# Optimization experiments

Measured on AMD Instinct MI355X. Metric: run time of the kernel, lower is better.

Reference implementation:

```python
import jax, jax.numpy as jnp
import numpy as np

T, N, B, D = 64, 8, 128, 128      # time, n_agents, batch, obs_dim
H, S, K, A = 512, 64, 16, 16       # hidden_dim, subtask_dim, num_subtasks, action_dim
NB = N * B


def setup_inputs() -> dict:
    key = jax.random.key(0)
    ks = jax.random.split(key, 16)
    r = lambda i, shape: jax.random.normal(ks[i], shape, jnp.float32) * 0.02
    return dict(
        h1=jnp.zeros((NB, H), jnp.float32),
        h2=jnp.zeros((NB, H), jnp.float32),
        obs=jax.random.normal(ks[0], (T, N, B, D), jnp.float32),
        done=jax.random.bernoulli(ks[1], 0.05, (T, NB)),
        W_embed=r(2, (D, H)), b_embed=jnp.zeros((H,), jnp.float32),
        Wi1=r(3, (H, 3 * H)), bi1=jnp.zeros((3 * H,), jnp.float32),
        Wh1=r(4, (H, 3 * H)), bhn1=jnp.zeros((H,), jnp.float32),
        W_sub=r(5, (H, S)), b_sub=jnp.zeros((S,), jnp.float32),
        W_e1=r(6, (K, S)), b_e1=jnp.zeros((S,), jnp.float32),
        W_e2=r(7, (S, S)), b_e2=jnp.zeros((S,), jnp.float32),
        W_pol=r(8, (D, H)), b_pol=jnp.zeros((H,), jnp.float32),
        Wi2=r(9, (H, 3 * H)), bi2=jnp.zeros((3 * H,), jnp.float32),
        Wh2=r(10, (H, 3 * H)), bhn2=jnp.zeros((H,), jnp.float32),
        W_w1=r(11, (S, H * A)), b_w1=jnp.zeros((H * A,), jnp.float32),
        W_b1=r(12, (S, A)), b_b1=jnp.zeros((A,), jnp.float32),
    )


def _gru(h0, xs, dones, Wi, bi, Wh, bhn):
    """Flax GRUCell with per-step reset-to-zero carry (ScannedRNN)."""
    def step(h, inp):
        x, d = inp
        h = jnp.where(d[:, None], 0.0, h)          # reset carry on done
        gi = x @ Wi + bi                            # (NB, 3H): ir|iz|in
        gh = h @ Wh                                 # (NB, 3H): hr|hz|hn (hn bias separate)
        ir, iz, inn = jnp.split(gi, 3, axis=-1)
        hr, hz, hn = jnp.split(gh, 3, axis=-1)
        rg = jax.nn.sigmoid(ir + hr)
        zg = jax.nn.sigmoid(iz + hz)
        ng = jnp.tanh(inn + rg * (hn + bhn))
        hnew = (1.0 - zg) * ng + zg * h
        return hnew, hnew
    return jax.lax.scan(step, h0, (xs, dones))


def reference(h1, h2, obs, done, W_embed, b_embed, Wi1, bi1, Wh1, bhn1,
              W_sub, b_sub, W_e1, b_e1, W_e2, b_e2, W_pol, b_pol,
              Wi2, bi2, Wh2, bhn2, W_w1, b_w1, W_b1, b_b1):
    t, n, b, _ = obs.shape
    obs_f = obs.reshape(t, n * b, -1)                       # (T, NB, D)

    # agent embedding branch + GRU 1
    ae = jax.nn.relu(obs_f @ W_embed + b_embed)             # (T, NB, H)
    hT1, y1 = _gru(h1, ae, done, Wi1, bi1, Wh1, bhn1)
    ae2 = y1 @ W_sub + b_sub                                # (T, NB, S)
    ae2 = jnp.transpose(ae2.reshape(t, n, b, S), (0, 2, 1, 3))  # (T, B, N, S)

    # subtask embedding: input is eye(K), identical over (t, b) -> compute once
    e = jnp.tanh(jax.nn.relu(jnp.eye(K, dtype=obs.dtype) @ W_e1 + b_e1) @ W_e2 + b_e2)  # (K, S)
    subtask_embed = jnp.broadcast_to(e, (t, b, K, S))

    subtask_logits = jnp.einsum('tbns,ks->tbnk', ae2, e)    # (T, B, N, K)
    subtask_prob = jax.nn.one_hot(jnp.argmax(subtask_logits, axis=-1), K, dtype=obs.dtype)  # eval path

    # subtask policy branch + GRU 2
    sp = jax.nn.relu(obs_f @ W_pol + b_pol)                 # (T, NB, H)
    hT2, y2 = _gru(h2, sp, done, Wi2, bi2, Wh2, bhn2)

    # hypernetwork: _subtask_embed = stop_grad(subtask_embed[:, 0]) == e (time-invariant)
    e_sg = jax.lax.stop_gradient(e)
    w1 = (e_sg @ W_w1 + b_w1).reshape(K, H, A)              # (K, H, A)
    b1 = e_sg @ W_b1 + b_b1                                 # (K, A)

    # equivalent to the repeated-w1 batched matmul, without materializing (T,NB*K,H,A)
    q = jnp.einsum('tbh,kha->tbka', y2, w1) + b1            # (T, NB, K, A), NB in (N,B)-major order

    # faithful to original: prob flattened (B,N)-major vs q flattened (N,B)-major
    prob_flat = subtask_prob.reshape(t, b * n, K)
    q_vals = jnp.einsum('tbk,tbka->tba', prob_flat, q)      # (T, NB, A)

    return ((hT1, hT2), q_vals, subtask_logits, subtask_embed)
```

## Files before the change

kernel.cpp:

```cpp
#include <hip/hip_runtime.h>
#include <hip/hip_bf16.h>
#include <math.h>

#define TT 64
#define NN 8
#define BB 128
#define DD 128
#define HH 512
#define SS 64
#define KK 16
#define AA 16
#define NB 1024
#define H3 (3*HH)

typedef float f4v  __attribute__((ext_vector_type(4)));
typedef float f16v __attribute__((ext_vector_type(16)));
typedef short bf16x8 __attribute__((ext_vector_type(8)));

__device__ __forceinline__ float sigm(float x){ return 1.0f/(1.0f+expf(-x)); }
__device__ __forceinline__ unsigned short f2bf(float f){
  unsigned u = __float_as_uint(f);
  u += 0x7FFF + ((u >> 16) & 1);
  return (unsigned short)(u >> 16);
}
__device__ __forceinline__ float bf2f(unsigned short h){
  return __uint_as_float(((unsigned)h) << 16);
}

__global__ __launch_bounds__(256) void k_detect(const unsigned char* __restrict__ raw,
                                                int* __restrict__ flag)
{
  __shared__ int cA, cB;
  if (threadIdx.x == 0){ cA = 0; cB = 0; }
  __syncthreads();
  int a = 0, b = 0;
  for (int i = threadIdx.x; i < TT*NB; i += 256){
    unsigned char v = raw[i];
    if (v > 1) a++;
    if ((i & 3) != 0 && v != 0) b++;
  }
  atomicAdd(&cA, a); atomicAdd(&cB, b);
  __syncthreads();
  if (threadIdx.x == 0) *flag = (cB == 0) ? 0 : (cA == 0 ? 1 : 2);
}

__global__ __launch_bounds__(256) void k_mask(const unsigned char* __restrict__ raw,
                                              const int* __restrict__ flag,
                                              float* __restrict__ mask)
{
  int i = blockIdx.x*256 + threadIdx.x;
  if (i >= TT*NB) return;
  int f = *flag;
  int v;
  if (f == 1)      v = (int)raw[i];
  else if (f == 0) v = ((const int*)raw)[i];
  else             v = (((const float*)raw)[i] != 0.0f);
  mask[i] = v ? 0.f : 1.f;
}


__global__ __launch_bounds__(256) void k_e(const float* __restrict__ W_e1, const float* __restrict__ b_e1,
                                           const float* __restrict__ W_e2, const float* __restrict__ b_e2,
                                           float* __restrict__ e_out)
{
  __shared__ float r1[KK*SS];
  int tid = threadIdx.x;
  for (int i=0;i<4;++i){ int l = tid + i*256; float v = W_e1[l] + b_e1[l & 63]; r1[l] = v > 0.f ? v : 0.f; }
  __syncthreads();
  for (int i=0;i<4;++i){
    int l = tid + i*256; int k = l >> 6, s = l & 63;
    float acc = b_e2[s];
    #pragma unroll 8
    for (int sp=0; sp<64; ++sp) acc += r1[k*64+sp] * W_e2[sp*64 + s];
    e_out[l] = tanhf(acc);
  }
}

__global__ __launch_bounds__(256) void k_w1b1(const float* __restrict__ e, const float* __restrict__ W_w1,
                                              const float* __restrict__ b_w1, const float* __restrict__ W_b1,
                                              const float* __restrict__ b_b1, float* __restrict__ w1,
                                              float* __restrict__ b1)
{
  __shared__ float es[KK*SS];
  int tid = threadIdx.x;
  for (int i=0;i<4;++i) es[tid + i*256] = e[tid + i*256];
  __syncthreads();
  for (int i=0;i<4;++i){
    int l = blockIdx.x*1024 + tid + i*256;
    int k = l >> 13, m = l & 8191;
    float acc = b_w1[m];
    #pragma unroll 8
    for (int s=0;s<64;++s) acc += es[k*64+s] * W_w1[(size_t)s*8192 + m];
    w1[l] = acc;
  }
  if (blockIdx.x == 0){
    int k = tid >> 4, a = tid & 15;
    float acc = b_b1[a];
    #pragma unroll 8
    for (int s=0;s<64;++s) acc += es[k*64+s] * W_b1[s*16 + a];
    b1[tid] = acc;
  }
}

__global__ __launch_bounds__(256) void k_se(const float* __restrict__ e, float* __restrict__ outse)
{
  __shared__ float4 es[256];
  es[threadIdx.x] = ((const float4*)e)[threadIdx.x];
  __syncthreads();
  const int total4 = TT*BB*KK*SS/4;
  for (int i = blockIdx.x*256 + threadIdx.x; i < total4; i += gridDim.x*256)
    ((float4*)outse)[i] = es[i & 255];
}

__global__ void k_copy(const float* __restrict__ src, float* __restrict__ dst, int n4)
{
  int i = blockIdx.x*blockDim.x + threadIdx.x;
  if (i < n4) ((float4*)dst)[i] = ((const float4*)src)[i];
}

__global__ void k_merge(const unsigned short* __restrict__ h, const unsigned short* __restrict__ l,
                        float* __restrict__ o, int n8)
{
  int i = blockIdx.x*blockDim.x + threadIdx.x;
  if (i >= n8) return;
  uint4 vh = *(const uint4*)&h[(size_t)i*8];
  uint4 vl = *(const uint4*)&l[(size_t)i*8];
  const unsigned short* ph = (const unsigned short*)&vh;
  const unsigned short* pl = (const unsigned short*)&vl;
  float4 o0, o1;
  o0.x = bf2f(ph[0])+bf2f(pl[0]); o0.y = bf2f(ph[1])+bf2f(pl[1]);
  o0.z = bf2f(ph[2])+bf2f(pl[2]); o0.w = bf2f(ph[3])+bf2f(pl[3]);
  o1.x = bf2f(ph[4])+bf2f(pl[4]); o1.y = bf2f(ph[5])+bf2f(pl[5]);
  o1.z = bf2f(ph[6])+bf2f(pl[6]); o1.w = bf2f(ph[7])+bf2f(pl[7]);
  float4* d = (float4*)&o[(size_t)i*8];
  d[0] = o0; d[1] = o1;
}

__global__ void k_expand(const unsigned short* __restrict__ src, float* __restrict__ dst, int n8)
{
  int i = blockIdx.x*blockDim.x + threadIdx.x;
  if (i >= n8) return;
  uint4 v = *(const uint4*)&src[(size_t)i*8];
  const unsigned short* p = (const unsigned short*)&v;
  float4 o0 = make_float4(bf2f(p[0]),bf2f(p[1]),bf2f(p[2]),bf2f(p[3]));
  float4 o1 = make_float4(bf2f(p[4]),bf2f(p[5]),bf2f(p[6]),bf2f(p[7]));
  float4* d = (float4*)&dst[(size_t)i*8];
  d[0] = o0; d[1] = o1;
}

__global__ void k_cast_bf16(const float* __restrict__ src, unsigned short* __restrict__ dst, int n8)
{
  int i = blockIdx.x*blockDim.x + threadIdx.x;
  if (i >= n8) return;
  const float4* s = (const float4*)(src + (size_t)i*8);
  float4 a = s[0], b = s[1];
  union { unsigned short u[8]; uint4 v; } p;
  p.u[0]=f2bf(a.x); p.u[1]=f2bf(a.y); p.u[2]=f2bf(a.z); p.u[3]=f2bf(a.w);
  p.u[4]=f2bf(b.x); p.u[5]=f2bf(b.y); p.u[6]=f2bf(b.z); p.u[7]=f2bf(b.w);
  *(uint4*)&dst[(size_t)i*8] = p.v;
}

__global__ __launch_bounds__(256) void k_tsplit(const float* __restrict__ W,
                                                unsigned short* __restrict__ WTh,
                                                unsigned short* __restrict__ WTl,
                                                int Kd, int Nc)
{
  __shared__ float t[32][33];
  int n0 = blockIdx.x * 32;
  int k0 = blockIdx.y * 32;
  int c = threadIdx.x & 31, r8 = threadIdx.x >> 5;
  for (int i=0;i<4;++i){
    int r = r8 + i*8;
    t[r][c] = W[(size_t)(k0+r)*Nc + n0 + c];
  }
  __syncthreads();
  for (int i=0;i<4;++i){
    int nr = r8 + i*8;
    float v = t[c][nr];
    unsigned short hi = f2bf(v);
    WTh[(size_t)(n0+nr)*Kd + k0 + c] = hi;
    WTl[(size_t)(n0+nr)*Kd + k0 + c] = f2bf(v - bf2f(hi));
  }
}

__global__ void k_split_cast(const float* __restrict__ src,
                             unsigned short* __restrict__ dh,
                             unsigned short* __restrict__ dl, int n8)
{
  int i = blockIdx.x*blockDim.x + threadIdx.x;
  if (i >= n8) return;
  const float4* s = (const float4*)(src + (size_t)i*8);
  float4 a = s[0], b = s[1];
  float x[8] = {a.x,a.y,a.z,a.w,b.x,b.y,b.z,b.w};
  union { unsigned short u[8]; uint4 v; } ph, pl;
  #pragma unroll
  for (int j=0;j<8;++j){
    unsigned short hi = f2bf(x[j]);
    ph.u[j] = hi;
    pl.u[j] = f2bf(x[j] - bf2f(hi));
  }
  *(uint4*)&dh[(size_t)i*8] = ph.v;
  *(uint4*)&dl[(size_t)i*8] = pl.v;
}

template<int KD, int SPLIT, int NTILE, int RELU, int OUTMODE>
__global__ __launch_bounds__(256) void mfma_gemm(
    const unsigned short* Ah, const unsigned short* Al,
    const unsigned short* Bh, const unsigned short* Bl,
    const float* __restrict__ bias,
    float* C, unsigned short* Chi, unsigned short* Clo, int Nstride)
{
  constexpr int NFC = NTILE/16;
  __shared__ __align__(16) unsigned short AsH[128*40];
  __shared__ __align__(16) unsigned short BsH[NTILE*40];
  __shared__ __align__(16) unsigned short AsL[SPLIT ? 128*40 : 8];
  __shared__ __align__(16) unsigned short BsL[SPLIT ? NTILE*40 : 8];
  int tid = threadIdx.x;
  int w = tid >> 6, l = tid & 63;
  int lr = l & 15, lk = (l >> 4) * 8, lq = l >> 4;
  int rowBase = blockIdx.y * 128, colBase = blockIdx.x * NTILE;
  f4v acc[2][NFC];
  f4v z = {0.f,0.f,0.f,0.f};
  #pragma unroll
  for (int i=0;i<2;++i)
    #pragma unroll
    for (int j=0;j<NFC;++j) acc[i][j] = z;

  for (int k0 = 0; k0 < KD; k0 += 32){
    {
      int r = tid >> 1, half = tid & 1;
      size_t src = (size_t)(rowBase + r)*KD + k0 + half*16;
      bf16x8* dA = (bf16x8*)&AsH[r*40 + half*16];
      dA[0] = *(const bf16x8*)&Ah[src];
      dA[1] = *(const bf16x8*)&Ah[src + 8];
      if (SPLIT){
        bf16x8* dL = (bf16x8*)&AsL[r*40 + half*16];
        dL[0] = *(const bf16x8*)&Al[src];
        dL[1] = *(const bf16x8*)&Al[src + 8];
      }
    }
    if (NTILE == 128){
      int r = tid >> 1, half = tid & 1;
      size_t src = (size_t)(colBase + r)*KD + k0 + half*16;
      bf16x8* dB = (bf16x8*)&BsH[r*40 + half*16];
      dB[0] = *(const bf16x8*)&Bh[src];
      dB[1] = *(const bf16x8*)&Bh[src + 8];
      if (SPLIT){
        bf16x8* dL = (bf16x8*)&BsL[r*40 + half*16];
        dL[0] = *(const bf16x8*)&Bl[src];
        dL[1] = *(const bf16x8*)&Bl[src + 8];
      }
    } else {
      int r = tid >> 2, q = tid & 3;
      size_t src = (size_t)(colBase + r)*KD + k0 + q*8;
      *(bf16x8*)&BsH[r*40 + q*8] = *(const bf16x8*)&Bh[src];
      if (SPLIT)
        *(bf16x8*)&BsL[r*40 + q*8] = *(const bf16x8*)&Bl[src];
    }
    __syncthreads();
    bf16x8 aH0 = *(const bf16x8*)&AsH[(w*32 + lr)*40 + lk];
    bf16x8 aH1 = *(const bf16x8*)&AsH[(w*32 + 16 + lr)*40 + lk];
    bf16x8 aL0, aL1;
    if (SPLIT){
      aL0 = *(const bf16x8*)&AsL[(w*32 + lr)*40 + lk];
      aL1 = *(const bf16x8*)&AsL[(w*32 + 16 + lr)*40 + lk];
    }
    #pragma unroll
    for (int fc=0; fc<NFC; ++fc){
      bf16x8 bH = *(const bf16x8*)&BsH[(fc*16 + lr)*40 + lk];
      acc[0][fc] = __builtin_amdgcn_mfma_f32_16x16x32_bf16(aH0, bH, acc[0][fc], 0,0,0);
      acc[1][fc] = __builtin_amdgcn_mfma_f32_16x16x32_bf16(aH1, bH, acc[1][fc], 0,0,0);
      if (SPLIT){
        bf16x8 bL = *(const bf16x8*)&BsL[(fc*16 + lr)*40 + lk];
        acc[0][fc] = __builtin_amdgcn_mfma_f32_16x16x32_bf16(aH0, bL, acc[0][fc], 0,0,0);
        acc[1][fc] = __builtin_amdgcn_mfma_f32_16x16x32_bf16(aH1, bL, acc[1][fc], 0,0,0);
        acc[0][fc] = __builtin_amdgcn_mfma_f32_16x16x32_bf16(aL0, bH, acc[0][fc], 0,0,0);
        acc[1][fc] = __builtin_amdgcn_mfma_f32_16x16x32_bf16(aL1, bH, acc[1][fc], 0,0,0);
      }
    }
    __syncthreads();
  }
  #pragma unroll
  for (int fr=0; fr<2; ++fr){
    #pragma unroll
    for (int fc=0; fc<NFC; ++fc){
      int col = colBase + fc*16 + lr;
      float bv = bias[col];
      #pragma unroll
      for (int r=0;r<4;++r){
        int row = rowBase + w*32 + fr*16 + lq*4 + r;
        float v = acc[fr][fc][r] + bv;
        if (RELU) v = v > 0.f ? v : 0.f;
        size_t o = (size_t)row*Nstride + col;
        if (OUTMODE == 0) C[o] = v;
        else if (OUTMODE == 1) Chi[o] = f2bf(v);
        else {
          unsigned short hi = f2bf(v);
          Chi[o] = hi;
          Clo[o] = f2bf(v - bf2f(hi));
        }
      }
    }
  }
}

__global__ __launch_bounds__(256) void gru_step_mix5(
    const unsigned short* __restrict__ hp1h, const unsigned short* __restrict__ hp1l,
    const unsigned short* __restrict__ hp2b,
    const float* __restrict__ gi1, const float* __restrict__ gi2,
    const unsigned short* __restrict__ Wh1TH, const unsigned short* __restrict__ Wh1TL,
    const unsigned short* __restrict__ Wh2T,
    const float* __restrict__ bhn1, const float* __restrict__ bhn2,
    const float* __restrict__ mask_t,
    unsigned short* __restrict__ y2b,
    unsigned short* __restrict__ y1h, unsigned short* __restrict__ y1l)
{
  extern __shared__ __align__(16) char smem[];
  int bid = blockIdx.x;
  int tid = threadIdx.x;
  int w = tid >> 6, l = tid & 63;
  int rf = w & 1, hc = w >> 1;
  int lc = l & 31, lh = l >> 5;
  int sr = tid >> 2, sg = tid & 3;
  int gru = bid & 1, sub = bid >> 1;
  int ct = sub & 7, rt = sub >> 3;
  int rowBase = rt << 6, colBase = ct << 6;
  int capchunk = ct*2 + hc;
  bool keep = mask_t[rowBase + sr] != 0.f;
  f16v z16 = {0,0,0,0,0,0,0,0,0,0,0,0,0,0,0,0};
  uint4 zero4 = {0,0,0,0};

  if (gru == 0){
    f16v acc[3] = {z16, z16, z16};
    float hval[16];
    uint4 pA;
    bf16x8 pB[3];
    pA = *(const uint4*)&hp2b[(size_t)(rowBase + sr)*HH + sg*8];
    #pragma unroll
    for (int i=0;i<3;++i){
      int unit = i*256 + tid, brow = unit >> 2, q = unit & 3;
      int g = brow >> 6, c = brow & 63;
      pB[i] = *(const bf16x8*)&Wh2T[(size_t)(g*HH + colBase + c)*HH + q*8];
    }
    {
      unsigned short* As0 = (unsigned short*)smem;
      unsigned short* Bs0 = As0 + 64*40;
      *(uint4*)&As0[sr*40 + sg*8] = keep ? pA : zero4;
      #pragma unroll
      for (int i=0;i<3;++i){
        int unit = i*256 + tid, brow = unit >> 2, q = unit & 3;
        *(bf16x8*)&Bs0[brow*40 + q*8] = pB[i];
      }
    }
    pA = *(const uint4*)&hp2b[(size_t)(rowBase + sr)*HH + 32 + sg*8];
    #pragma unroll
    for (int i=0;i<3;++i){
      int unit = i*256 + tid, brow = unit >> 2, q = unit & 3;
      int g = brow >> 6, c = brow & 63;
      pB[i] = *(const bf16x8*)&Wh2T[(size_t)(g*HH + colBase + c)*HH + 32 + q*8];
    }
    __syncthreads();
    for (int ck = 0; ck < 16; ++ck){
      unsigned short* Asc = (unsigned short*)(smem + (ck&1)*20480);
      unsigned short* Bsc = Asc + 64*40;
      if (ck < 15){
        unsigned short* Asn = (unsigned short*)(smem + ((ck+1)&1)*20480);
        unsigned short* Bsn = Asn + 64*40;
        *(uint4*)&Asn[sr*40 + sg*8] = keep ? pA : zero4;
        #pragma unroll
        for (int i=0;i<3;++i){
          int unit = i*256 + tid, brow = unit >> 2, q = unit & 3;
          *(bf16x8*)&Bsn[brow*40 + q*8] = pB[i];
        }
      }
      if (ck < 14){
        int k0 = (ck+2)*32;
        pA = *(const uint4*)&hp2b[(size_t)(rowBase + sr)*HH + k0 + sg*8];
        #pragma unroll
        for (int i=0;i<3;++i){
          int unit = i*256 + tid, brow = unit >> 2, q = unit & 3;
          int g = brow >> 6, c = brow & 63;
          pB[i] = *(const bf16x8*)&Wh2T[(size_t)(g*HH + colBase + c)*HH + k0 + q*8];
        }
      }
      if (ck == capchunk){
        #pragma unroll
        for (int r=0;r<16;++r){
          int rl = rf*32 + (r&3) + 8*(r>>2) + 4*lh;
          hval[r] = bf2f(Asc[rl*40 + lc]);
        }
      }
      #pragma unroll
      for (int kc=0;kc<32;kc+=16){
        bf16x8 a = *(const bf16x8*)&Asc[(rf*32 + lc)*40 + kc + lh*8];
        #pragma unroll
        for (int g=0; g<3; ++g){
          bf16x8 b = *(const bf16x8*)&Bsc[(g*64 + hc*32 + lc)*40 + kc + lh*8];
          acc[g] = __builtin_amdgcn_mfma_f32_32x32x16_bf16(a, b, acc[g], 0,0,0);
        }
      }
      __syncthreads();
    }
    int col = colBase + hc*32 + lc;
    float bn = bhn2[col];
    #pragma unroll
    for (int r=0;r<16;++r){
      int row = rowBase + rf*32 + (r&3) + 8*(r>>2) + 4*lh;
      size_t gb = (size_t)row*H3 + col;
      float g_r = __builtin_nontemporal_load(&gi2[gb]);
      float g_z = __builtin_nontemporal_load(&gi2[gb + HH]);
      float g_n = __builtin_nontemporal_load(&gi2[gb + 2*HH]);
      float rg = sigm(g_r + acc[0][r]);
      float zg = sigm(g_z + acc[1][r]);
      float ng = tanhf(g_n + rg*(acc[2][r] + bn));
      float o  = (1.f - zg)*ng + zg*hval[r];
      y2b[(size_t)row*HH + col] = f2bf(o);
    }
  } else {
    f16v acc[3] = {z16, z16, z16};
    float hval[16];
    uint4 pAh, pAl;
    bf16x8 pBH[3], pBL[3];
    pAh = *(const uint4*)&hp1h[(size_t)(rowBase + sr)*HH + sg*8];
    pAl = *(const uint4*)&hp1l[(size_t)(rowBase + sr)*HH + sg*8];
    #pragma unroll
    for (int i=0;i<3;++i){
      int unit = i*256 + tid, brow = unit >> 2, q = unit & 3;
      int g = brow >> 6, c = brow & 63;
      size_t src = (size_t)(g*HH + colBase + c)*HH + q*8;
      pBH[i] = *(const bf16x8*)&Wh1TH[src];
      pBL[i] = *(const bf16x8*)&Wh1TL[src];
    }
    {
      unsigned short* AsH0 = (unsigned short*)smem;
      unsigned short* AsL0 = AsH0 + 64*40;
      unsigned short* BsH0 = AsL0 + 64*40;
      unsigned short* BsL0 = BsH0 + 192*40;
      *(uint4*)&AsH0[sr*40 + sg*8] = keep ? pAh : zero4;
      *(uint4*)&AsL0[sr*40 + sg*8] = keep ? pAl : zero4;
      #pragma unroll
      for (int i=0;i<3;++i){
        int unit = i*256 + tid, brow = unit >> 2, q = unit & 3;
        *(bf16x8*)&BsH0[brow*40 + q*8] = pBH[i];
        *(bf16x8*)&BsL0[brow*40 + q*8] = pBL[i];
      }
    }
    pAh = *(const uint4*)&hp1h[(size_t)(rowBase + sr)*HH + 32 + sg*8];
    pAl = *(const uint4*)&hp1l[(size_t)(rowBase + sr)*HH + 32 + sg*8];
    #pragma unroll
    for (int i=0;i<3;++i){
      int unit = i*256 + tid, brow = unit >> 2, q = unit & 3;
      int g = brow >> 6, c = brow & 63;
      size_t src = (size_t)(g*HH + colBase + c)*HH + 32 + q*8;
      pBH[i] = *(const bf16x8*)&Wh1TH[src];
      pBL[i] = *(const bf16x8*)&Wh1TL[src];
    }
    __syncthreads();
    for (int ck = 0; ck < 16; ++ck){
      unsigned short* AsHc = (unsigned short*)(smem + (ck&1)*40960);
      unsigned short* AsLc = AsHc + 64*40;
      unsigned short* BsHc = AsLc + 64*40;
      unsigned short* BsLc = BsHc + 192*40;
      if (ck < 15){
        unsigned short* AsHn = (unsigned short*)(smem + ((ck+1)&1)*40960);
        unsigned short* AsLn = AsHn + 64*40;
        unsigned short* BsHn = AsLn + 64*40;
        unsigned short* BsLn = BsHn + 192*40;
        *(uint4*)&AsHn[sr*40 + sg*8] = keep ? pAh : zero4;
        *(uint4*)&AsLn[sr*40 + sg*8] = keep ? pAl : zero4;
        #pragma unroll
        for (int i=0;i<3;++i){
          int unit = i*256 + tid, brow = unit >> 2, q = unit & 3;
          *(bf16x8*)&BsHn[brow*40 + q*8] = pBH[i];
          *(bf16x8*)&BsLn[brow*40 + q*8] = pBL[i];
        }
      }
      if (ck < 14){
        int k0 = (ck+2)*32;
        pAh = *(const uint4*)&hp1h[(size_t)(rowBase + sr)*HH + k0 + sg*8];
        pAl = *(const uint4*)&hp1l[(size_t)(rowBase + sr)*HH + k0 + sg*8];
        #pragma unroll
        for (int i=0;i<3;++i){
          int unit = i*256 + tid, brow = unit >> 2, q = unit & 3;
          int g = brow >> 6, c = brow & 63;
          size_t src = (size_t)(g*HH + colBase + c)*HH + k0 + q*8;
          pBH[i] = *(const bf16x8*)&Wh1TH[src];
          pBL[i] = *(const bf16x8*)&Wh1TL[src];
        }
      }
      if (ck == capchunk){
        #pragma unroll
        for (int r=0;r<16;++r){
          int rl = rf*32 + (r&3) + 8*(r>>2) + 4*lh;
          hval[r] = bf2f(AsHc[rl*40 + lc]) + bf2f(AsLc[rl*40 + lc]);
        }
      }
      #pragma unroll
      for (int kc=0;kc<32;kc+=16){
        bf16x8 aH = *(const bf16x8*)&AsHc[(rf*32 + lc)*40 + kc + lh*8];
        bf16x8 aL = *(const bf16x8*)&AsLc[(rf*32 + lc)*40 + kc + lh*8];
        #pragma unroll
        for (int g=0; g<3; ++g){
          int brow = (g*64 + hc*32 + lc)*40 + kc + lh*8;
          bf16x8 bH = *(const bf16x8*)&BsHc[brow];
          bf16x8 bL = *(const bf16x8*)&BsLc[brow];
          acc[g] = __builtin_amdgcn_mfma_f32_32x32x16_bf16(aH, bH, acc[g], 0,0,0);
          acc[g] = __builtin_amdgcn_mfma_f32_32x32x16_bf16(aH, bL, acc[g], 0,0,0);
          acc[g] = __builtin_amdgcn_mfma_f32_32x32x16_bf16(aL, bH, acc[g], 0,0,0);
        }
      }
      __syncthreads();
    }
    int col = colBase + hc*32 + lc;
    float bn = bhn1[col];
    #pragma unroll
    for (int r=0;r<16;++r){
      int row = rowBase + rf*32 + (r&3) + 8*(r>>2) + 4*lh;
      size_t gb = (size_t)row*H3 + col;
      float g_r = __builtin_nontemporal_load(&gi1[gb]);
      float g_z = __builtin_nontemporal_load(&gi1[gb + HH]);
      float g_n = __builtin_nontemporal_load(&gi1[gb + 2*HH]);
      float rg = sigm(g_r + acc[0][r]);
      float zg = sigm(g_z + acc[1][r]);
      float ng = tanhf(g_n + rg*(acc[2][r] + bn));
      float o  = (1.f - zg)*ng + zg*hval[r];
      size_t oo = (size_t)row*HH + col;
      unsigned short hi = f2bf(o);
      y1h[oo] = hi;
      y1l[oo] = f2bf(o - bf2f(hi));
    }
  }
}

__global__ __launch_bounds__(256) void k_logits(const float* __restrict__ ae2,
    const float* __restrict__ e, float* __restrict__ out_logits, int* __restrict__ argk, int t0)
{
  __shared__ float es[KK*SS];
  int tid = threadIdx.x;
  for (int i=0;i<4;++i) es[tid + i*256] = e[tid + i*256];
  __syncthreads();
  int g = blockIdx.x*256 + tid;
  int t = t0 + (g >> 10), j = g & 1023;
  const float* arow = &ae2[(size_t)g * SS];
  float a[SS];
  #pragma unroll
  for (int i=0;i<16;++i){ float4 v = ((const float4*)arow)[i]; a[4*i]=v.x; a[4*i+1]=v.y; a[4*i+2]=v.z; a[4*i+3]=v.w; }
  float lg[KK];
  float best = -INFINITY; int bk = 0;
  #pragma unroll
  for (int k=0;k<KK;++k){
    float s2 = 0.f;
    #pragma unroll
    for (int s=0;s<SS;++s) s2 += a[s]*es[k*SS+s];
    lg[k] = s2;
    if (s2 > best){ best = s2; bk = k; }
  }
  int n = j >> 7, b = j & 127;
  size_t ob = ((size_t)((t*BB + b)*NN + n)) * KK;
  #pragma unroll
  for (int k4=0;k4<4;++k4)
    *(float4*)&out_logits[ob + k4*4] = make_float4(lg[k4*4],lg[k4*4+1],lg[k4*4+2],lg[k4*4+3]);
  argk[(t*BB + b)*NN + n] = bk;
}

__global__ __launch_bounds__(64) void k_qsel(const unsigned short* __restrict__ y2b,
    const float* __restrict__ w1, const float* __restrict__ b1,
    const int* __restrict__ argk, float* __restrict__ outq)
{
  __shared__ float yr[HH];
  __shared__ float part[64];
  int bj = blockIdx.x;
  int tid = threadIdx.x;
  {
    uint4 v = *(const uint4*)&y2b[(size_t)bj*HH + tid*8];
    const unsigned short* p = (const unsigned short*)&v;
    #pragma unroll
    for (int j=0;j<8;++j) yr[tid*8 + j] = bf2f(p[j]);
  }
  __syncthreads();
  int k = argk[bj];
  int a = tid & 15, q4 = tid >> 4;
  const float* wp = &w1[(size_t)k*HH*AA + a];
  float s = 0.f;
  int h0 = q4*128;
  #pragma unroll 8
  for (int h=h0; h<h0+128; ++h) s += yr[h]*wp[(size_t)h*AA];
  part[tid] = s;
  __syncthreads();
  if (q4 == 0){
    float v = part[a] + part[a+16] + part[a+32] + part[a+48] + b1[k*AA + a];
    outq[(size_t)bj*AA + a] = v;
  }
}

extern "C" void kernel_launch(void* const* d_in, const int* in_sizes, int n_in,
                              void* d_out, int out_size, void* d_ws, size_t ws_size,
                              hipStream_t stream)
{
  (void)in_sizes; (void)n_in; (void)out_size;
  const float* h1     = (const float*)d_in[0];
  const float* h2     = (const float*)d_in[1];
  const float* obs    = (const float*)d_in[2];
  const unsigned char* done_raw = (const unsigned char*)d_in[3];
  const float* W_embed=(const float*)d_in[4];  const float* b_embed=(const float*)d_in[5];
  const float* Wi1    =(const float*)d_in[6];  const float* bi1    =(const float*)d_in[7];
  const float* Wh1    =(const float*)d_in[8];  const float* bhn1   =(const float*)d_in[9];
  const float* W_sub  =(const float*)d_in[10]; const float* b_sub  =(const float*)d_in[11];
  const float* W_e1   =(const float*)d_in[12]; const float* b_e1   =(const float*)d_in[13];
  const float* W_e2   =(const float*)d_in[14]; const float* b_e2   =(const float*)d_in[15];
  const float* W_pol  =(const float*)d_in[16]; const float* b_pol  =(const float*)d_in[17];
  const float* Wi2    =(const float*)d_in[18]; const float* bi2    =(const float*)d_in[19];
  const float* Wh2    =(const float*)d_in[20]; const float* bhn2   =(const float*)d_in[21];
  const float* W_w1   =(const float*)d_in[22]; const float* b_w1   =(const float*)d_in[23];
  const float* W_b1   =(const float*)d_in[24]; const float* b_b1   =(const float*)d_in[25];

  float* out    = (float*)d_out;
  float* outHT1 = out;
  float* outHT2 = out + (size_t)NB*HH;
  float* outQ   = out + 2ull*NB*HH;
  float* outLG  = outQ + (size_t)TT*NB*AA;
  float* outSE  = outLG + (size_t)TT*BB*NN*KK;

  const size_t fixed_f = (size_t)TT*NB + 1024
                       + (size_t)KK*HH*AA + 256 + (size_t)TT*NB + 64
                       + 2ull*NB*HH/2
                       + (size_t)NB*HH/2
                       + 2ull*DD*HH/2 * 2
                       + 4ull*H3*HH
                       + (size_t)HH*SS;
  const size_t per_t_f = (size_t)NB*(2*H3 + SS)
                       + (size_t)NB*(HH/2 + DD + HH + HH/2);
  int CH = 64;
  while (CH > 1 && (fixed_f + per_t_f*(size_t)CH)*4 > ws_size) CH >>= 1;

  float* gbuf1  = (float*)d_ws;
  float* gbuf2  = gbuf1  + (size_t)CH*NB*H3;
  float* ae2buf = gbuf2  + (size_t)CH*NB*H3;
  float* maskp  = ae2buf + (size_t)CH*NB*SS;
  float* ws_e   = maskp  + (size_t)TT*NB;
  float* ws_w1  = ws_e   + 1024;
  float* ws_b1  = ws_w1  + (size_t)KK*HH*AA;
  int*   ws_argk= (int*)(ws_b1 + 256);
  int*   ws_flag= (int*)(ws_argk + (size_t)TT*NB);
  unsigned short* buf2bf = (unsigned short*)(ws_flag + 64);
  unsigned short* obs_h  = buf2bf + (size_t)CH*NB*HH;
  unsigned short* obs_l  = obs_h  + (size_t)CH*NB*DD;
  unsigned short* y1_h   = obs_l  + (size_t)CH*NB*DD;
  unsigned short* y1_l   = y1_h   + (size_t)CH*NB*HH;
  unsigned short* y2b    = y1_l   + (size_t)CH*NB*HH;
  unsigned short* hl1h   = y2b    + (size_t)CH*NB*HH;
  unsigned short* hl1l   = hl1h   + (size_t)NB*HH;
  unsigned short* h2b0   = hl1l   + (size_t)NB*HH;
  unsigned short* wembt_h= h2b0   + (size_t)NB*HH;
  unsigned short* wembt_l= wembt_h+ (size_t)HH*DD;
  unsigned short* wpolt_h= wembt_l+ (size_t)HH*DD;
  unsigned short* wpolt_l= wpolt_h+ (size_t)HH*DD;
  unsigned short* wi1t_h = wpolt_l+ (size_t)HH*DD;
  unsigned short* wi1t_l = wi1t_h + (size_t)H3*HH;
  unsigned short* wi2t_h = wi1t_l + (size_t)H3*HH;
  unsigned short* wi2t_l = wi2t_h + (size_t)H3*HH;
  unsigned short* wh1t_h = wi2t_l + (size_t)H3*HH;
  unsigned short* wh1t_l = wh1t_h + (size_t)H3*HH;
  unsigned short* wh2t_h = wh1t_l + (size_t)H3*HH;
  unsigned short* wh2t_l = wh2t_h + (size_t)H3*HH;
  unsigned short* wsubt_h= wh2t_l + (size_t)H3*HH;
  unsigned short* wsubt_l= wsubt_h+ (size_t)SS*HH;

  hipFuncSetAttribute((const void*)gru_step_mix5,
                      hipFuncAttributeMaxDynamicSharedMemorySize, 81920);

  k_detect<<<1,256,0,stream>>>(done_raw, ws_flag);
  k_mask<<<TT*NB/256,256,0,stream>>>(done_raw, ws_flag, maskp);
  k_e<<<1,256,0,stream>>>(W_e1,b_e1,W_e2,b_e2,ws_e);
  k_w1b1<<<128,256,0,stream>>>(ws_e,W_w1,b_w1,W_b1,b_b1,ws_w1,ws_b1);
  k_se<<<2048,256,0,stream>>>(ws_e,outSE);
  k_tsplit<<<dim3(16,4),256,0,stream>>>(W_embed, wembt_h, wembt_l, DD, HH);
  k_tsplit<<<dim3(16,4),256,0,stream>>>(W_pol,   wpolt_h, wpolt_l, DD, HH);
  k_tsplit<<<dim3(48,16),256,0,stream>>>(Wi1, wi1t_h, wi1t_l, HH, H3);
  k_tsplit<<<dim3(48,16),256,0,stream>>>(Wi2, wi2t_h, wi2t_l, HH, H3);
  k_tsplit<<<dim3(48,16),256,0,stream>>>(Wh1, wh1t_h, wh1t_l, HH, H3);
  k_tsplit<<<dim3(48,16),256,0,stream>>>(Wh2, wh2t_h, wh2t_l, HH, H3);
  k_tsplit<<<dim3(2,16),256,0,stream>>>(W_sub, wsubt_h, wsubt_l, HH, SS);
  k_split_cast<<<NB*HH/8/256,256,0,stream>>>(h1, hl1h, hl1l, NB*HH/8);
  k_cast_bf16<<<NB*HH/8/256,256,0,stream>>>(h2, h2b0, NB*HH/8);

  dim3 thr(256);
  const int NCH = TT / CH;
  for (int c = 0; c < NCH; ++c){
    int t0 = c * CH;
    int M = CH*NB;
    const float* obs_c = obs + (size_t)t0*NB*DD;
    k_split_cast<<<(M*DD/8+255)/256,256,0,stream>>>(obs_c, obs_h, obs_l, M*DD/8);
    mfma_gemm<DD,1,128,1,2><<<dim3(HH/128, M/128),thr,0,stream>>>(
        obs_h, obs_l, wembt_h, wembt_l, b_embed, nullptr, y1_h, y1_l, HH);
    mfma_gemm<HH,1,128,0,0><<<dim3(H3/128, M/128),thr,0,stream>>>(
        y1_h, y1_l, wi1t_h, wi1t_l, bi1, gbuf1, nullptr, nullptr, H3);
    mfma_gemm<DD,0,128,1,1><<<dim3(HH/128, M/128),thr,0,stream>>>(
        obs_h, obs_h, wpolt_h, wpolt_h, b_pol, nullptr, buf2bf, nullptr, HH);
    mfma_gemm<HH,0,128,0,0><<<dim3(H3/128, M/128),thr,0,stream>>>(
        buf2bf, buf2bf, wi2t_h, wi2t_h, bi2, gbuf2, nullptr, nullptr, H3);
    for (int lt = 0; lt < CH; ++lt){
      const unsigned short* hp1h = (lt == 0) ? hl1h : (y1_h + (size_t)(lt-1)*NB*HH);
      const unsigned short* hp1l = (lt == 0) ? hl1l : (y1_l + (size_t)(lt-1)*NB*HH);
      const unsigned short* hp2b = (c == 0 && lt == 0) ? h2b0 :
                                   (lt == 0 ? y2b + (size_t)(CH-1)*NB*HH
                                            : y2b + (size_t)(lt-1)*NB*HH);
      gru_step_mix5<<<256, 256, 81920, stream>>>(hp1h, hp1l, hp2b,
                                                 gbuf1 + (size_t)lt*NB*H3, gbuf2 + (size_t)lt*NB*H3,
                                                 wh1t_h, wh1t_l, wh2t_h, bhn1, bhn2,
                                                 maskp + (size_t)(t0+lt)*NB,
                                                 y2b + (size_t)lt*NB*HH,
                                                 y1_h + (size_t)lt*NB*HH, y1_l + (size_t)lt*NB*HH);
    }
    k_copy<<<256,256,0,stream>>>((const float*)(y1_h + (size_t)(CH-1)*NB*HH), (float*)hl1h, NB*HH/8);
    k_copy<<<256,256,0,stream>>>((const float*)(y1_l + (size_t)(CH-1)*NB*HH), (float*)hl1l, NB*HH/8);
    mfma_gemm<HH,1,64,0,0><<<dim3(1, M/128),thr,0,stream>>>(
        y1_h, y1_l, wsubt_h, wsubt_l, b_sub, ae2buf, nullptr, nullptr, SS);
    k_logits<<<M/256,256,0,stream>>>(ae2buf, ws_e, outLG, ws_argk, t0);
    k_qsel<<<M,64,0,stream>>>(y2b, ws_w1, ws_b1, ws_argk + (size_t)t0*NB, outQ + (size_t)t0*NB*AA);
  }
  k_merge<<<NB*HH/8/256,256,0,stream>>>(hl1h, hl1l, outHT1, NB*HH/8);
  k_expand<<<NB*HH/8/256,256,0,stream>>>(y2b + (size_t)(CH-1)*NB*HH, outHT2, NB*HH/8);
}
```

Measured before the change: 2.987 ms.

## Double GRU step K-chunk to 64 and drop per-chunk hidden-state copies

The recurrent GRU step kernel now stages 64-wide K chunks instead of 32, halving the number of loop iterations and barriers per step. The LDS row stride becomes 72, double buffers grow to about 144KB, and launch bounds force one block per CU. Embedding outputs move to a separate ae_h/ae_l buffer so y1 holds only GRU1 outputs across chunks, which removes the k_copy of the last hidden state and lets the final merge read directly from y1. This costs extra workspace, which may shrink the time-chunk size CH, and limits occupancy to one block per CU.

```diff
diff --git a/kernel.cpp b/kernel.cpp
--- a/kernel.cpp
+++ b/kernel.cpp
@@ -12,6 +12,9 @@
 #define AA 16
 #define NB 1024
 #define H3 (3*HH)
+
+#define SCAN_BUF_SHORTS 36864
+#define SCAN_SMEM (2*SCAN_BUF_SHORTS*2)
 
 typedef float f4v  __attribute__((ext_vector_type(4)));
 typedef float f16v __attribute__((ext_vector_type(16)));
@@ -304,7 +307,7 @@
   }
 }
 
-__global__ __launch_bounds__(256) void gru_step_mix5(
+__global__ __launch_bounds__(256, 1) void gru_step_mix6(
     const unsigned short* __restrict__ hp1h, const unsigned short* __restrict__ hp1l,
     const unsigned short* __restrict__ hp2b,
     const float* __restrict__ gi1, const float* __restrict__ gi2,
@@ -315,87 +318,86 @@
     unsigned short* __restrict__ y2b,
     unsigned short* __restrict__ y1h, unsigned short* __restrict__ y1l)
 {
-  extern __shared__ __align__(16) char smem[];
+  extern __shared__ __align__(16) unsigned short smem[];
   int bid = blockIdx.x;
   int tid = threadIdx.x;
   int w = tid >> 6, l = tid & 63;
   int rf = w & 1, hc = w >> 1;
   int lc = l & 31, lh = l >> 5;
-  int sr = tid >> 2, sg = tid & 3;
   int gru = bid & 1, sub = bid >> 1;
   int ct = sub & 7, rt = sub >> 3;
   int rowBase = rt << 6, colBase = ct << 6;
-  int capchunk = ct*2 + hc;
-  bool keep = mask_t[rowBase + sr] != 0.f;
+  int capchunk = ct, capoff = hc*32;
+  int ar0 = tid >> 3, aq = tid & 7;
+  int ar1 = ar0 + 32;
+  bool keep0 = mask_t[rowBase + ar0] != 0.f;
+  bool keep1 = mask_t[rowBase + ar1] != 0.f;
   f16v z16 = {0,0,0,0,0,0,0,0,0,0,0,0,0,0,0,0};
   uint4 zero4 = {0,0,0,0};
+
+  size_t asrc0 = (size_t)(rowBase + ar0)*HH + aq*8;
+  size_t asrc1 = (size_t)(rowBase + ar1)*HH + aq*8;
+  size_t bsrc[6];
+  #pragma unroll
+  for (int i=0;i<6;++i){
+    int brow = i*32 + ar0;
+    bsrc[i] = (size_t)((brow>>6)*HH + colBase + (brow&63))*HH + aq*8;
+  }
+  int adst0 = ar0*72 + aq*8, adst1 = ar1*72 + aq*8;
+  int bdst[6];
+  #pragma unroll
+  for (int i=0;i<6;++i) bdst[i] = (i*32 + ar0)*72 + aq*8;
 
   if (gru == 0){
     f16v acc[3] = {z16, z16, z16};
     float hval[16];
-    uint4 pA;
-    bf16x8 pB[3];
-    pA = *(const uint4*)&hp2b[(size_t)(rowBase + sr)*HH + sg*8];
-    #pragma unroll
-    for (int i=0;i<3;++i){
-      int unit = i*256 + tid, brow = unit >> 2, q = unit & 3;
-      int g = brow >> 6, c = brow & 63;
-      pB[i] = *(const bf16x8*)&Wh2T[(size_t)(g*HH + colBase + c)*HH + q*8];
-    }
+    uint4 pA0, pA1;
+    bf16x8 pB[6];
+    pA0 = *(const uint4*)&hp2b[asrc0];  pA1 = *(const uint4*)&hp2b[asrc1];
+    #pragma unroll
+    for (int i=0;i<6;++i) pB[i] = *(const bf16x8*)&Wh2T[bsrc[i]];
     {
-      unsigned short* As0 = (unsigned short*)smem;
-      unsigned short* Bs0 = As0 + 64*40;
-      *(uint4*)&As0[sr*40 + sg*8] = keep ? pA : zero4;
+      unsigned short* As = smem;
+      unsigned short* Bs = smem + 4608;
+      *(uint4*)&As[adst0] = keep0 ? pA0 : zero4;
+      *(uint4*)&As[adst1] = keep1 ? pA1 : zero4;
       #pragma unroll
-      for (int i=0;i<3;++i){
-        int unit = i*256 + tid, brow = unit >> 2, q = unit & 3;
-        *(bf16x8*)&Bs0[brow*40 + q*8] = pB[i];
-      }
-    }
-    pA = *(const uint4*)&hp2b[(size_t)(rowBase + sr)*HH + 32 + sg*8];
-    #pragma unroll
-    for (int i=0;i<3;++i){
-      int unit = i*256 + tid, brow = unit >> 2, q = unit & 3;
-      int g = brow >> 6, c = brow & 63;
-      pB[i] = *(const bf16x8*)&Wh2T[(size_t)(g*HH + colBase + c)*HH + 32 + q*8];
-    }
+      for (int i=0;i<6;++i) *(bf16x8*)&Bs[bdst[i]] = pB[i];
+    }
+    pA0 = *(const uint4*)&hp2b[asrc0 + 64];  pA1 = *(const uint4*)&hp2b[asrc1 + 64];
+    #pragma unroll
+    for (int i=0;i<6;++i) pB[i] = *(const bf16x8*)&Wh2T[bsrc[i] + 64];
     __syncthreads();
-    for (int ck = 0; ck < 16; ++ck){
-      unsigned short* Asc = (unsigned short*)(smem + (ck&1)*20480);
-      unsigned short* Bsc = Asc + 64*40;
-      if (ck < 15){
-        unsigned short* Asn = (unsigned short*)(smem + ((ck+1)&1)*20480);
-        unsigned short* Bsn = Asn + 64*40;
-        *(uint4*)&Asn[sr*40 + sg*8] = keep ? pA : zero4;
+    for (int ck = 0; ck < 8; ++ck){
+      if (ck < 7){
+        unsigned short* As = smem + ((ck+1)&1)*SCAN_BUF_SHORTS;
+        unsigned short* Bs = As + 4608;
+        *(uint4*)&As[adst0] = keep0 ? pA0 : zero4;
+        *(uint4*)&As[adst1] = keep1 ? pA1 : zero4;
         #pragma unroll
-        for (int i=0;i<3;++i){
-          int unit = i*256 + tid, brow = unit >> 2, q = unit & 3;
-          *(bf16x8*)&Bsn[brow*40 + q*8] = pB[i];
-        }
-      }
-      if (ck < 14){
-        int k0 = (ck+2)*32;
-        pA = *(const uint4*)&hp2b[(size_t)(rowBase + sr)*HH + k0 + sg*8];
+        for (int i=0;i<6;++i) *(bf16x8*)&Bs[bdst[i]] = pB[i];
+      }
+      if (ck < 6){
+        int k0 = (ck+2)*64;
+        pA0 = *(const uint4*)&hp2b[asrc0 + k0];  pA1 = *(const uint4*)&hp2b[asrc1 + k0];
         #pragma unroll
-        for (int i=0;i<3;++i){
-          int unit = i*256 + tid, brow = unit >> 2, q = unit & 3;
-          int g = brow >> 6, c = brow & 63;
-          pB[i] = *(const bf16x8*)&Wh2T[(size_t)(g*HH + colBase + c)*HH + k0 + q*8];
-        }
-      }
+        for (int i=0;i<6;++i) pB[i] = *(const bf16x8*)&Wh2T[bsrc[i] + k0];
+      }
+      unsigned short* Asc = smem + (ck&1)*SCAN_BUF_SHORTS;
+      unsigned short* Bsc = Asc + 4608;
       if (ck == capchunk){
         #pragma unroll
         for (int r=0;r<16;++r){
           int rl = rf*32 + (r&3) + 8*(r>>2) + 4*lh;
-          hval[r] = bf2f(Asc[rl*40 + lc]);
+          hval[r] = bf2f(Asc[rl*72 + capoff + lc]);
         }
       }
       #pragma unroll
-      for (int kc=0;kc<32;kc+=16){
-        bf16x8 a = *(const bf16x8*)&Asc[(rf*32 + lc)*40 + kc + lh*8];
+      for (int kc=0;kc<64;kc+=16){
+        bf16x8 a = *(const bf16x8*)&Asc[(rf*32 + lc)*72 + kc + lh*8];
         #pragma unroll
         for (int g=0; g<3; ++g){
-          bf16x8 b = *(const bf16x8*)&Bsc[(g*64 + hc*32 + lc)*40 + kc + lh*8];
+          bf16x8 b = *(const bf16x8*)&Bsc[(g*64 + hc*32 + lc)*72 + kc + lh*8];
           acc[g] = __builtin_amdgcn_mfma_f32_32x32x16_bf16(a, b, acc[g], 0,0,0);
         }
       }
@@ -419,91 +421,69 @@
   } else {
     f16v acc[3] = {z16, z16, z16};
     float hval[16];
-    uint4 pAh, pAl;
-    bf16x8 pBH[3], pBL[3];
-    pAh = *(const uint4*)&hp1h[(size_t)(rowBase + sr)*HH + sg*8];
-    pAl = *(const uint4*)&hp1l[(size_t)(rowBase + sr)*HH + sg*8];
-    #pragma unroll
-    for (int i=0;i<3;++i){
-      int unit = i*256 + tid, brow = unit >> 2, q = unit & 3;
-      int g = brow >> 6, c = brow & 63;
-      size_t src = (size_t)(g*HH + colBase + c)*HH + q*8;
-      pBH[i] = *(const bf16x8*)&Wh1TH[src];
-      pBL[i] = *(const bf16x8*)&Wh1TL[src];
-    }
+    uint4 pAh0, pAh1, pAl0, pAl1;
+    bf16x8 pBH[6], pBL[6];
+    pAh0 = *(const uint4*)&hp1h[asrc0];  pAh1 = *(const uint4*)&hp1h[asrc1];
+    pAl0 = *(const uint4*)&hp1l[asrc0];  pAl1 = *(const uint4*)&hp1l[asrc1];
+    #pragma unroll
+    for (int i=0;i<6;++i){ pBH[i] = *(const bf16x8*)&Wh1TH[bsrc[i]]; pBL[i] = *(const bf16x8*)&Wh1TL[bsrc[i]]; }
     {
-      unsigned short* AsH0 = (unsigned short*)smem;
-      unsigned short* AsL0 = AsH0 + 64*40;
-      unsigned short* BsH0 = AsL0 + 64*40;
-      unsigned short* BsL0 = BsH0 + 192*40;
-      *(uint4*)&AsH0[sr*40 + sg*8] = keep ? pAh : zero4;
-      *(uint4*)&AsL0[sr*40 + sg*8] = keep ? pAl : zero4;
+      unsigned short* AsH = smem;
+      unsigned short* AsL = smem + 4608;
+      unsigned short* BsH = smem + 9216;
+      unsigned short* BsL = smem + 23040;
+      *(uint4*)&AsH[adst0] = keep0 ? pAh0 : zero4;
+      *(uint4*)&AsH[adst1] = keep1 ? pAh1 : zero4;
+      *(uint4*)&AsL[adst0] = keep0 ? pAl0 : zero4;
+      *(uint4*)&AsL[adst1] = keep1 ? pAl1 : zero4;
       #pragma unroll
-      for (int i=0;i<3;++i){
-        int unit = i*256 + tid, brow = unit >> 2, q = unit & 3;
-        *(bf16x8*)&BsH0[brow*40 + q*8] = pBH[i];
-        *(bf16x8*)&BsL0[brow*40 + q*8] = pBL[i];
-      }
-    }
-    pAh = *(const uint4*)&hp1h[(size_t)(rowBase + sr)*HH + 32 + sg*8];
-    pAl = *(const uint4*)&hp1l[(size_t)(rowBase + sr)*HH + 32 + sg*8];
-    #pragma unroll
-    for (int i=0;i<3;++i){
-      int unit = i*256 + tid, brow = unit >> 2, q = unit & 3;
-      int g = brow >> 6, c = brow & 63;
-      size_t src = (size_t)(g*HH + colBase + c)*HH + 32 + q*8;
-      pBH[i] = *(const bf16x8*)&Wh1TH[src];
-      pBL[i] = *(const bf16x8*)&Wh1TL[src];
-    }
+      for (int i=0;i<6;++i){ *(bf16x8*)&BsH[bdst[i]] = pBH[i]; *(bf16x8*)&BsL[bdst[i]] = pBL[i]; }
+    }
+    pAh0 = *(const uint4*)&hp1h[asrc0 + 64];  pAh1 = *(const uint4*)&hp1h[asrc1 + 64];
+    pAl0 = *(const uint4*)&hp1l[asrc0 + 64];  pAl1 = *(const uint4*)&hp1l[asrc1 + 64];
+    #pragma unroll
+    for (int i=0;i<6;++i){ pBH[i] = *(const bf16x8*)&Wh1TH[bsrc[i] + 64]; pBL[i] = *(const bf16x8*)&Wh1TL[bsrc[i] + 64]; }
     __syncthreads();
-    for (int ck = 0; ck < 16; ++ck){
-      unsigned short* AsHc = (unsigned short*)(smem + (ck&1)*40960);
-      unsigned short* AsLc = AsHc + 64*40;
-      unsigned short* BsHc = AsLc + 64*40;
-      unsigned short* BsLc = BsHc + 192*40;
-      if (ck < 15){
-        unsigned short* AsHn = (unsigned short*)(smem + ((ck+1)&1)*40960);
-        unsigned short* AsLn = AsHn + 64*40;
-        unsigned short* BsHn = AsLn + 64*40;
-        unsigned short* BsLn = BsHn + 192*40;
-        *(uint4*)&AsHn[sr*40 + sg*8] = keep ? pAh : zero4;
-        *(uint4*)&AsLn[sr*40 + sg*8] = keep ? pAl : zero4;
+    for (int ck = 0; ck < 8; ++ck){
+      if (ck < 7){
+        unsigned short* AsH = smem + ((ck+1)&1)*SCAN_BUF_SHORTS;
+        unsigned short* AsL = AsH + 4608;
+        unsigned short* BsH = AsH + 9216;
+        unsigned short* BsL = AsH + 23040;
+        *(uint4*)&AsH[adst0] = keep0 ? pAh0 : zero4;
+        *(uint4*)&AsH[adst1] = keep1 ? pAh1 : zero4;
+        *(uint4*)&AsL[adst0] = keep0 ? pAl0 : zero4;
+        *(uint4*)&AsL[adst1] = keep1 ? pAl1 : zero4;
         #pragma unroll
-        for (int i=0;i<3;++i){
-          int unit = i*256 + tid, brow = unit >> 2, q = unit & 3;
-          *(bf16x8*)&BsHn[brow*40 + q*8] = pBH[i];
-          *(bf16x8*)&BsLn[brow*40 + q*8] = pBL[i];
-        }
-      }
-      if (ck < 14){
-        int k0 = (ck+2)*32;
-        pAh = *(const uint4*)&hp1h[(size_t)(rowBase + sr)*HH + k0 + sg*8];
-        pAl = *(const uint4*)&hp1l[(size_t)(rowBase + sr)*HH + k0 + sg*8];
+        for (int i=0;i<6;++i){ *(bf16x8*)&BsH[bdst[i]] = pBH[i]; *(bf16x8*)&BsL[bdst[i]] = pBL[i]; }
+      }
+      if (ck < 6){
+        int k0 = (ck+2)*64;
+        pAh0 = *(const uint4*)&hp1h[asrc0 + k0];  pAh1 = *(const uint4*)&hp1h[asrc1 + k0];
+        pAl0 = *(const uint4*)&hp1l[asrc0 + k0];  pAl1 = *(const uint4*)&hp1l[asrc1 + k0];
         #pragma unroll
-        for (int i=0;i<3;++i){
-          int unit = i*256 + tid, brow = unit >> 2, q = unit & 3;
-          int g = brow >> 6, c = brow & 63;
-          size_t src = (size_t)(g*HH + colBase + c)*HH + k0 + q*8;
-          pBH[i] = *(const bf16x8*)&Wh1TH[src];
-          pBL[i] = *(const bf16x8*)&Wh1TL[src];
-        }
-      }
+        for (int i=0;i<6;++i){ pBH[i] = *(const bf16x8*)&Wh1TH[bsrc[i] + k0]; pBL[i] = *(const bf16x8*)&Wh1TL[bsrc[i] + k0]; }
+      }
+      unsigned short* AsHc = smem + (ck&1)*SCAN_BUF_SHORTS;
+      unsigned short* AsLc = AsHc + 4608;
+      unsigned short* BsHc = AsHc + 9216;
+      unsigned short* BsLc = AsHc + 23040;
       if (ck == capchunk){
         #pragma unroll
         for (int r=0;r<16;++r){
           int rl = rf*32 + (r&3) + 8*(r>>2) + 4*lh;
-          hval[r] = bf2f(AsHc[rl*40 + lc]) + bf2f(AsLc[rl*40 + lc]);
+          hval[r] = bf2f(AsHc[rl*72 + capoff + lc]) + bf2f(AsLc[rl*72 + capoff + lc]);
         }
       }
       #pragma unroll
-      for (int kc=0;kc<32;kc+=16){
-        bf16x8 aH = *(const bf16x8*)&AsHc[(rf*32 + lc)*40 + kc + lh*8];
-        bf16x8 aL = *(const bf16x8*)&AsLc[(rf*32 + lc)*40 + kc + lh*8];
+      for (int kc=0;kc<64;kc+=16){
+        bf16x8 aH = *(const bf16x8*)&AsHc[(rf*32 + lc)*72 + kc + lh*8];
+        bf16x8 aL = *(const bf16x8*)&AsLc[(rf*32 + lc)*72 + kc + lh*8];
         #pragma unroll
         for (int g=0; g<3; ++g){
-          int brow = (g*64 + hc*32 + lc)*40 + kc + lh*8;
-          bf16x8 bH = *(const bf16x8*)&BsHc[brow];
-          bf16x8 bL = *(const bf16x8*)&BsLc[brow];
+          int bro = (g*64 + hc*32 + lc)*72 + kc + lh*8;
+          bf16x8 bH = *(const bf16x8*)&BsHc[bro];
+          bf16x8 bL = *(const bf16x8*)&BsLc[bro];
           acc[g] = __builtin_amdgcn_mfma_f32_32x32x16_bf16(aH, bH, acc[g], 0,0,0);
           acc[g] = __builtin_amdgcn_mfma_f32_32x32x16_bf16(aH, bL, acc[g], 0,0,0);
           acc[g] = __builtin_amdgcn_mfma_f32_32x32x16_bf16(aL, bH, acc[g], 0,0,0);
@@ -629,7 +609,7 @@
                        + 4ull*H3*HH
                        + (size_t)HH*SS;
   const size_t per_t_f = (size_t)NB*(2*H3 + SS)
-                       + (size_t)NB*(HH/2 + DD + HH + HH/2);
+                       + (size_t)NB*(HH/2 + DD + HH + HH/2 + HH);
   int CH = 64;
   while (CH > 1 && (fixed_f + per_t_f*(size_t)CH)*4 > ws_size) CH >>= 1;
 
@@ -648,7 +628,9 @@
   unsigned short* y1_h   = obs_l  + (size_t)CH*NB*DD;
   unsigned short* y1_l   = y1_h   + (size_t)CH*NB*HH;
   unsigned short* y2b    = y1_l   + (size_t)CH*NB*HH;
-  unsigned short* hl1h   = y2b    + (size_t)CH*NB*HH;
+  unsigned short* ae_h   = y2b    + (size_t)CH*NB*HH;
+  unsigned short* ae_l   = ae_h   + (size_t)CH*NB*HH;
+  unsigned short* hl1h   = ae_l   + (size_t)CH*NB*HH;
   unsigned short* hl1l   = hl1h   + (size_t)NB*HH;
   unsigned short* h2b0   = hl1l   + (size_t)NB*HH;
   unsigned short* wembt_h= h2b0   + (size_t)NB*HH;
@@ -666,8 +648,8 @@
   unsigned short* wsubt_h= wh2t_l + (size_t)H3*HH;
   unsigned short* wsubt_l= wsubt_h+ (size_t)SS*HH;
 
-  hipFuncSetAttribute((const void*)gru_step_mix5,
-                      hipFuncAttributeMaxDynamicSharedMemorySize, 81920);
+  hipFuncSetAttribute((const void*)gru_step_mix6,
+                      hipFuncAttributeMaxDynamicSharedMemorySize, SCAN_SMEM);
 
   k_detect<<<1,256,0,stream>>>(done_raw, ws_flag);
   k_mask<<<TT*NB/256,256,0,stream>>>(done_raw, ws_flag, maskp);
@@ -692,33 +674,32 @@
     const float* obs_c = obs + (size_t)t0*NB*DD;
     k_split_cast<<<(M*DD/8+255)/256,256,0,stream>>>(obs_c, obs_h, obs_l, M*DD/8);
     mfma_gemm<DD,1,128,1,2><<<dim3(HH/128, M/128),thr,0,stream>>>(
-        obs_h, obs_l, wembt_h, wembt_l, b_embed, nullptr, y1_h, y1_l, HH);
+        obs_h, obs_l, wembt_h, wembt_l, b_embed, nullptr, ae_h, ae_l, HH);
     mfma_gemm<HH,1,128,0,0><<<dim3(H3/128, M/128),thr,0,stream>>>(
-        y1_h, y1_l, wi1t_h, wi1t_l, bi1, gbuf1, nullptr, nullptr, H3);
+        ae_h, ae_l, wi1t_h, wi1t_l, bi1, gbuf1, nullptr, nullptr, H3);
     mfma_gemm<DD,0,128,1,1><<<dim3(HH/128, M/128),thr,0,stream>>>(
         obs_h, obs_h, wpolt_h, wpolt_h, b_pol, nullptr, buf2bf, nullptr, HH);
     mfma_gemm<HH,0,128,0,0><<<dim3(H3/128, M/128),thr,0,stream>>>(
         buf2bf, buf2bf, wi2t_h, wi2t_h, bi2, gbuf2, nullptr, nullptr, H3);
     for (int lt = 0; lt < CH; ++lt){
-      const unsigned short* hp1h = (lt == 0) ? hl1h : (y1_h + (size_t)(lt-1)*NB*HH);
-      const unsigned short* hp1l = (lt == 0) ? hl1l : (y1_l + (size_t)(lt-1)*NB*HH);
-      const unsigned short* hp2b = (c == 0 && lt == 0) ? h2b0 :
-                                   (lt == 0 ? y2b + (size_t)(CH-1)*NB*HH
-                                            : y2b + (size_t)(lt-1)*NB*HH);
-      gru_step_mix5<<<256, 256, 81920, stream>>>(hp1h, hp1l, hp2b,
-                                                 gbuf1 + (size_t)lt*NB*H3, gbuf2 + (size_t)lt*NB*H3,
-                                                 wh1t_h, wh1t_l, wh2t_h, bhn1, bhn2,
-                                                 maskp + (size_t)(t0+lt)*NB,
-                                                 y2b + (size_t)lt*NB*HH,
-                                                 y1_h + (size_t)lt*NB*HH, y1_l + (size_t)lt*NB*HH);
-    }
-    k_copy<<<256,256,0,stream>>>((const float*)(y1_h + (size_t)(CH-1)*NB*HH), (float*)hl1h, NB*HH/8);
-    k_copy<<<256,256,0,stream>>>((const float*)(y1_l + (size_t)(CH-1)*NB*HH), (float*)hl1l, NB*HH/8);
+      const unsigned short* hp1h = (lt == 0) ? (c == 0 ? hl1h : y1_h + (size_t)(CH-1)*NB*HH)
+                                             : (y1_h + (size_t)(lt-1)*NB*HH);
+      const unsigned short* hp1l = (lt == 0) ? (c == 0 ? hl1l : y1_l + (size_t)(CH-1)*NB*HH)
+                                             : (y1_l + (size_t)(lt-1)*NB*HH);
+      const unsigned short* hp2b = (lt == 0) ? (c == 0 ? h2b0 : y2b + (size_t)(CH-1)*NB*HH)
+                                             : (y2b + (size_t)(lt-1)*NB*HH);
+      gru_step_mix6<<<256, 256, SCAN_SMEM, stream>>>(hp1h, hp1l, hp2b,
+                                                     gbuf1 + (size_t)lt*NB*H3, gbuf2 + (size_t)lt*NB*H3,
+                                                     wh1t_h, wh1t_l, wh2t_h, bhn1, bhn2,
+                                                     maskp + (size_t)(t0+lt)*NB,
+                                                     y2b + (size_t)lt*NB*HH,
+                                                     y1_h + (size_t)lt*NB*HH, y1_l + (size_t)lt*NB*HH);
+    }
     mfma_gemm<HH,1,64,0,0><<<dim3(1, M/128),thr,0,stream>>>(
         y1_h, y1_l, wsubt_h, wsubt_l, b_sub, ae2buf, nullptr, nullptr, SS);
     k_logits<<<M/256,256,0,stream>>>(ae2buf, ws_e, outLG, ws_argk, t0);
     k_qsel<<<M,64,0,stream>>>(y2b, ws_w1, ws_b1, ws_argk + (size_t)t0*NB, outQ + (size_t)t0*NB*AA);
   }
-  k_merge<<<NB*HH/8/256,256,0,stream>>>(hl1h, hl1l, outHT1, NB*HH/8);
+  k_merge<<<NB*HH/8/256,256,0,stream>>>(y1_h + (size_t)(CH-1)*NB*HH, y1_l + (size_t)(CH-1)*NB*HH, outHT1, NB*HH/8);
   k_expand<<<NB*HH/8/256,256,0,stream>>>(y2b + (size_t)(CH-1)*NB*HH, outHT2, NB*HH/8);
 }
```

After: 2.990 ms. Within noise of the previous version (+0.1%).
